# Performance work log

Hardware: AMD Instinct MI355X
Metric: run time of the kernel (lower is better)

The kernel has to match this reference:

```python
import jax, jax.numpy as jnp
import numpy as np

RANK_W, SP_W, ANS_W = 1.0, 1.0, 1.0


def _listmle(thres, scores, labels):
    # thres [B,1], scores [B,P], labels [B,P] with values in {-1,0,1}
    fs = jnp.concatenate([thres, scores], axis=1)                      # [B,K]
    fl = jnp.concatenate([jnp.full_like(thres, 0.5), labels], axis=1)  # [B,K]
    s = jnp.exp(fs) * (fl != -1.0).astype(fs.dtype)
    # rest[b,j] = sum_k s[b,k] * (fl[b,k] < fl[b,j])  (sorting in the original
    # is only used to enumerate; with the 0.5 break it reduces to masking
    # entries with label >= 0.5)
    less = (fl[:, None, :] < fl[:, :, None]).astype(fs.dtype)          # [B,j,k]
    rest = jnp.einsum('bjk,bk->bj', less, s)
    mask = fl >= 0.5
    den = jnp.where(mask, s + rest, 1.0)
    logp = jnp.where(mask, fs - jnp.log(den), 0.0)  # log(s_j/(s_j+rest)) with s_j=exp(fs_j)
    return -jnp.sum(logp)


def setup_inputs() -> dict:
    key = jax.random.key(0)
    B, S, H, NS, NP, A = 8, 4096, 1024, 64, 32, 8
    ks = jax.random.split(key, 12)
    sequence_output = jax.random.normal(ks[0], (B, S, H), jnp.float32)
    token_type_ids = jax.random.randint(ks[1], (B, S), 0, 2).astype(jnp.int32)
    # strictly increasing sentence boundaries; last 4 sentences padded with -1
    base = jnp.round(jnp.linspace(8, S - 8, NS + 1)).astype(jnp.int32)
    sent_starts = jnp.broadcast_to(base, (B, NS + 1)).copy()
    sent_starts = sent_starts.at[:, -4:].set(-1)
    para_starts = jnp.sort(jax.random.randint(ks[2], (B, NP), 0, S), axis=1).astype(jnp.int32)
    para_labels = jax.random.randint(ks[3], (B, NP), -1, 2).astype(jnp.float32)
    sp_sent_labels = jax.random.randint(ks[4], (B, NS), -1, 2).astype(jnp.float32)
    starts = jax.random.randint(ks[5], (B, A), -1, S).astype(jnp.int32)
    ends = jax.random.randint(ks[6], (B, A), -1, S).astype(jnp.int32)
    Wqa = jax.random.normal(ks[7], (H, 2), jnp.float32) * 0.02
    bqa = jnp.zeros((2,), jnp.float32)
    Wrank = jax.random.normal(ks[8], (H, 1), jnp.float32) * 0.02
    brank = jnp.zeros((1,), jnp.float32)
    Wsp = jax.random.normal(ks[9], (H, 1), jnp.float32) * 0.02
    bsp = jnp.zeros((1,), jnp.float32)
    return {"sequence_output": sequence_output, "token_type_ids": token_type_ids,
            "sent_starts": sent_starts, "para_starts": para_starts,
            "para_labels": para_labels, "sp_sent_labels": sp_sent_labels,
            "starts": starts, "ends": ends, "Wqa": Wqa, "bqa": bqa,
            "Wrank": Wrank, "brank": brank, "Wsp": Wsp, "bsp": bsp}


def reference(sequence_output, token_type_ids, sent_starts, para_starts,
              para_labels, sp_sent_labels, starts, ends,
              Wqa, bqa, Wrank, brank, Wsp, bsp):
    B, S, H = sequence_output.shape
    logits = sequence_output @ Wqa + bqa                               # [B,S,2]
    tt1 = token_type_ids == 1
    start_logits = jnp.where(tt1, logits[..., 0], -jnp.inf)
    end_logits = jnp.where(tt1, logits[..., 1], -jnp.inf)

    rank_thres = sequence_output[:, 0, :] @ Wrank + brank              # [B,1]
    sent_thres = sequence_output[:, 0, :] @ Wsp + bsp                  # [B,1]

    # ragged per-sentence mean pooling via prefix sums
    csum = jnp.concatenate([jnp.zeros((B, 1, H), sequence_output.dtype),
                            jnp.cumsum(sequence_output, axis=1)], axis=1)  # [B,S+1,H]
    st = sent_starts[:, :-1]
    en = sent_starts[:, 1:]
    valid = en != -1                                                   # [B,NS]
    st_c = jnp.clip(st, 0, S)
    en_c = jnp.maximum(jnp.clip(en, 0, S), st_c + 1)
    NS = st.shape[1]
    g_en = jnp.take_along_axis(csum, jnp.broadcast_to(en_c[:, :, None], (B, NS, H)), axis=1)
    g_st = jnp.take_along_axis(csum, jnp.broadcast_to(st_c[:, :, None], (B, NS, H)), axis=1)
    seg_mean = (g_en - g_st) / (en_c - st_c)[:, :, None].astype(sequence_output.dtype)
    sent_rep = jnp.where(valid[:, :, None], seg_mean, sequence_output[:, -1:, :])
    sp_score = (sent_rep @ Wsp + bsp)[..., 0]                          # [B,NS]

    NP = para_starts.shape[1]
    para_rep = jnp.take_along_axis(
        sequence_output, jnp.broadcast_to(para_starts[:, :, None].astype(jnp.int32), (B, NP, H)), axis=1)
    para_score = (para_rep @ Wrank + brank)[..., 0]                    # [B,NP]

    rank_loss = _listmle(rank_thres, para_score, para_labels)
    sp_loss = _listmle(sent_thres, sp_score, sp_sent_labels)

    ls_start = jax.nn.log_softmax(start_logits, axis=-1)
    ls_end = jax.nn.log_softmax(end_logits, axis=-1)

    def ce(ls, tgt):  # CrossEntropy with ignore_index=-1, reduction='none'
        safe = jnp.clip(tgt, 0, S - 1)
        nll = -jnp.take_along_axis(ls, safe, axis=1)
        return jnp.where(tgt == -1, 0.0, nll)

    loss_tensor = ce(ls_start, starts) + ce(ls_end, ends)              # [B,A]
    lp = -loss_tensor
    lp = jnp.where(lp == 0.0, -jnp.inf, lp)
    m = jnp.sum(jnp.exp(lp), axis=1)                                   # [B]
    pos = m > 0
    span_loss = -jnp.sum(jnp.where(pos, jnp.log(jnp.where(pos, m, 1.0)), 0.0))

    loss = rank_loss * RANK_W + span_loss * ANS_W + sp_loss * SP_W
    return (loss, rank_loss * RANK_W, sp_loss * SP_W)
```

## Files before the change

### kernel.cpp

```cpp
#include <hip/hip_runtime.h>
#include <math.h>

#define B 8
#define S 4096
#define H 1024
#define NSEG 64
#define NPARA 32
#define NA 8
#define BS (B * S)
#define ROWS_PER_BLK 16
#define BLKS_PER_B (S / ROWS_PER_BLK)
#define NBLK (B * BLKS_PER_B)

__device__ __forceinline__ float2 lse_merge(float2 A, float2 Bv)
{
    float m = fmaxf(A.x, Bv.x);
    float s = 0.f;
    if (A.y > 0.f)  s += A.y * expf(A.x - m);
    if (Bv.y > 0.f) s += Bv.y * expf(Bv.x - m);
    return make_float2(m, s);
}

__global__ __launch_bounds__(256) void dots_kernel(
    const float4* __restrict__ seq4,
    const float4* __restrict__ Wqa4,
    const float4* __restrict__ Wsp4,
    const float4* __restrict__ Wrank4,
    const int*    __restrict__ tt,
    const int*    __restrict__ sent_starts,
    float4* __restrict__ sc4,
    float4* __restrict__ lse_part,
    float4* __restrict__ segpart,
    float*  __restrict__ out)
{
    const int blk   = blockIdx.x;
    const int b     = blk >> 8;
    const int rbase = (blk & 255) * ROWS_PER_BLK;
    const int t     = threadIdx.x;
    const int w     = t >> 6, lane = t & 63;

    if (blk == 0 && t == 0) { out[0] = 0.f; out[1] = 0.f; out[2] = 0.f; }

    __shared__ int    ssh[NSEG + 1];
    __shared__ int    rowseg[ROWS_PER_BLK];
    __shared__ int    ttsh[ROWS_PER_BLK];
    __shared__ float4 lsep[4];
    __shared__ float2 wacc[4];
    __shared__ int    jlo_sh;

    float4 qA[4], qB[4], spv[4], rkv[4];
#pragma unroll
    for (int c = 0; c < 4; ++c) {
        const int ch = lane + 64 * c;
        qA[c]  = Wqa4[ch * 2];
        qB[c]  = Wqa4[ch * 2 + 1];
        spv[c] = Wsp4[ch];
        rkv[c] = Wrank4[ch];
    }

    if (t < NSEG + 1) ssh[t] = sent_starts[b * (NSEG + 1) + t];
    __syncthreads();
    if (t < ROWS_PER_BLK) {
        ttsh[t] = tt[b * S + rbase + t];
        const int r = rbase + t;
        int j = -1;
        for (int k = 0; k < NSEG; ++k) {
            int en = ssh[k + 1];
            if (en == -1) break;
            if (r >= ssh[k] && r < en) { j = k; break; }
        }
        rowseg[t] = j;
    }
    __syncthreads();
    if (t == 0) {
        int jl = -1;
        for (int i = 0; i < ROWS_PER_BLK; ++i)
            if (rowseg[i] >= 0) { jl = rowseg[i]; break; }
        jlo_sh = jl;
    }
    __syncthreads();
    const int jlo = jlo_sh;

    const float4* base = seq4 + (size_t)(b * S + rbase) * (H / 4);
    float mm = -INFINITY, ssum = 0.f;
    float segA = 0.f, segB = 0.f;

#pragma unroll
    for (int g = 0; g < 4; ++g) {
        const int lrow = g * 4 + w;
        const float4* rp = base + (size_t)lrow * (H / 4);
        float a0 = 0.f, a1 = 0.f, a2 = 0.f, a3 = 0.f;
#pragma unroll
        for (int c = 0; c < 4; ++c) {
            float4 v = rp[lane + 64 * c];
            a0 += v.x * qA[c].x + v.y * qA[c].z + v.z * qB[c].x + v.w * qB[c].z;
            a1 += v.x * qA[c].y + v.y * qA[c].w + v.z * qB[c].y + v.w * qB[c].w;
            a2 += v.x * spv[c].x + v.y * spv[c].y + v.z * spv[c].z + v.w * spv[c].w;
            a3 += v.x * rkv[c].x + v.y * rkv[c].y + v.z * rkv[c].z + v.w * rkv[c].w;
        }
        float u01 = (lane & 1) ? a0 : a1;
        float x01 = ((lane & 1) ? a1 : a0) + __shfl_xor(u01, 1);
        float u23 = (lane & 1) ? a2 : a3;
        float x23 = ((lane & 1) ? a3 : a2) + __shfl_xor(u23, 1);
        float uu  = (lane & 2) ? x01 : x23;
        float x   = ((lane & 2) ? x23 : x01) + __shfl_xor(uu, 2);
#pragma unroll
        for (int off = 4; off < 64; off <<= 1) x += __shfl_xor(x, off);
        if (ttsh[lrow] == 1) {
            float mn = fmaxf(mm, x);
            ssum = ssum * expf(mm - mn) + expf(x - mn);
            mm = mn;
        }
        const int j = rowseg[lrow];
        if (j >= 0) { if (j == jlo) segA += x; else segB += x; }
        if (lane < 4)
            ((float*)(sc4 + (size_t)b * S + rbase + lrow))[lane] = x;
    }

    {
        float mE = __shfl(mm, 1),   sE = __shfl(ssum, 1);
        float sa = __shfl(segA, 2), sb = __shfl(segB, 2);
        if (lane == 0) {
            lsep[w] = make_float4(mm, ssum, mE, sE);
            wacc[w] = make_float2(sa, sb);
        }
    }
    __syncthreads();
    if (t == 0) {
        float2 L0 = make_float2(lsep[0].x, lsep[0].y);
        float2 L1 = make_float2(lsep[0].z, lsep[0].w);
        float SA = wacc[0].x, SB = wacc[0].y;
#pragma unroll
        for (int i = 1; i < 4; ++i) {
            L0 = lse_merge(L0, make_float2(lsep[i].x, lsep[i].y));
            L1 = lse_merge(L1, make_float2(lsep[i].z, lsep[i].w));
            SA += wacc[i].x; SB += wacc[i].y;
        }
        lse_part[blk] = make_float4(L0.x, L0.y, L1.x, L1.y);
        segpart[blk]  = make_float4(__int_as_float(jlo), SA, SB, 0.f);
    }
}

__device__ __forceinline__ float blk_reduce1(float v, float* wred1, int t)
{
    const int lane = t & 63, w = t >> 6;
#pragma unroll
    for (int off = 32; off > 0; off >>= 1) v += __shfl_xor(v, off);
    if (lane == 0) wred1[w] = v;
    __syncthreads();
    float r = wred1[0] + wred1[1] + wred1[2] + wred1[3];
    __syncthreads();
    return r;
}

__device__ float listmle_block(const float* fs, const float* fl, float* se,
                               int n, float* wred1, int t)
{
    if (t < n) se[t] = (fl[t] != -1.0f) ? expf(fs[t]) : 0.0f;
    __syncthreads();
    float lp = 0.0f;
    if (t < n && fl[t] >= 0.5f) {
        float fj = fl[t];
        float rest = 0.0f;
        for (int k = 0; k < n; ++k)
            if (fl[k] < fj) rest += se[k];
        lp = fs[t] - logf(se[t] + rest);
    }
    float tot = blk_reduce1(lp, wred1, t);
    return -tot;
}

__global__ __launch_bounds__(256) void batch_kernel(
    const float4* __restrict__ sc4,
    const float4* __restrict__ lse_part,
    const float4* __restrict__ segpart,
    const int*    __restrict__ tt,
    const int*    __restrict__ sent_starts,
    const int*    __restrict__ para_starts,
    const float*  __restrict__ para_labels,
    const float*  __restrict__ sp_labels,
    const int*    __restrict__ starts,
    const int*    __restrict__ ends,
    float* __restrict__ out)
{
    const int b = blockIdx.x;
    const int t = threadIdx.x;
    const int lane = t & 63, w = t >> 6;

    __shared__ float4 lsew[4];
    __shared__ float  segsum[NSEG + 2];
    __shared__ int    ssh[NSEG + 1];
    __shared__ float  wred1[4];
    __shared__ float  fsb[1 + NSEG], flb[1 + NSEG], seb[1 + NSEG];
    __shared__ float  lse_sh[2];

    const float4* sb  = sc4 + (size_t)b * S;
    const int*    ttb = tt + b * S;

    if (t < NSEG + 2) segsum[t] = 0.f;
    if (t < NSEG + 1) ssh[t] = sent_starts[b * (NSEG + 1) + t];
    __syncthreads();

    {
        float4 P = lse_part[(size_t)b * BLKS_PER_B + t];
        float2 L0 = make_float2(P.x, P.y);
        float2 L1 = make_float2(P.z, P.w);
#pragma unroll
        for (int off = 32; off > 0; off >>= 1) {
            float2 O0 = make_float2(__shfl_xor(L0.x, off), __shfl_xor(L0.y, off));
            float2 O1 = make_float2(__shfl_xor(L1.x, off), __shfl_xor(L1.y, off));
            L0 = lse_merge(L0, O0);
            L1 = lse_merge(L1, O1);
        }
        if (lane == 0) lsew[w] = make_float4(L0.x, L0.y, L1.x, L1.y);

        float4 SP = segpart[(size_t)b * BLKS_PER_B + t];
        int jl = __float_as_int(SP.x);
        if (jl >= 0) {
            atomicAdd(&segsum[jl], SP.y);
            atomicAdd(&segsum[jl + 1], SP.z);
        }
    }
    __syncthreads();
    if (t == 0) {
        float2 M0 = make_float2(lsew[0].x, lsew[0].y);
        float2 M1 = make_float2(lsew[0].z, lsew[0].w);
#pragma unroll
        for (int i = 1; i < 4; ++i) {
            M0 = lse_merge(M0, make_float2(lsew[i].x, lsew[i].y));
            M1 = lse_merge(M1, make_float2(lsew[i].z, lsew[i].w));
        }
        lse_sh[0] = M0.x + logf(M0.y);
        lse_sh[1] = M1.x + logf(M1.y);
    }

    if (t == 0) { fsb[0] = sb[0].z; flb[0] = 0.5f; }
    if (t < NSEG) {
        int st = ssh[t];
        int en = ssh[t + 1];
        float score;
        if (en != -1) {
            int stc = min(max(st, 0), S);
            int enc = max(min(max(en, 0), S), stc + 1);
            score = segsum[t] / (float)(enc - stc);
        } else {
            score = sb[S - 1].z;
        }
        fsb[1 + t] = score;
        flb[1 + t] = sp_labels[b * NSEG + t];
    }
    __syncthreads();
    float sp_loss_b = listmle_block(fsb, flb, seb, 1 + NSEG, wred1, t);

    if (t == 0) { fsb[0] = sb[0].w; flb[0] = 0.5f; }
    if (t < NPARA) {
        int ps = para_starts[b * NPARA + t];
        fsb[1 + t] = sb[ps].w;
        flb[1 + t] = para_labels[b * NPARA + t];
    }
    __syncthreads();
    float rank_loss_b = listmle_block(fsb, flb, seb, 1 + NPARA, wred1, t);

    float e_a = 0.f;
    if (t < NA) {
        const float lse0 = lse_sh[0], lse1 = lse_sh[1];
        int tsv = starts[b * NA + t];
        int tev = ends[b * NA + t];
        float lt = 0.f;
        if (tsv != -1) {
            int sf = min(max(tsv, 0), S - 1);
            float sl = (ttb[sf] == 1) ? sb[sf].x : -INFINITY;
            lt += -(sl - lse0);
        }
        if (tev != -1) {
            int sf = min(max(tev, 0), S - 1);
            float el = (ttb[sf] == 1) ? sb[sf].y : -INFINITY;
            lt += -(el - lse1);
        }
        float lp = -lt;
        e_a = (lp == 0.0f) ? 0.f : expf(lp);
    }
#pragma unroll
    for (int off = 4; off > 0; off >>= 1) e_a += __shfl_xor(e_a, off, 8);
    if (t == 0) {
        float logm = (e_a > 0.f) ? logf(e_a) : 0.f;
        atomicAdd(out + 0, rank_loss_b + sp_loss_b - logm);
        atomicAdd(out + 1, rank_loss_b);
        atomicAdd(out + 2, sp_loss_b);
    }
}

extern "C" void kernel_launch(void* const* d_in, const int* in_sizes, int n_in,
                              void* d_out, int out_size, void* d_ws, size_t ws_size,
                              hipStream_t stream)
{
    const float* seq         = (const float*)d_in[0];
    const int*   tt          = (const int*)  d_in[1];
    const int*   sent_starts = (const int*)  d_in[2];
    const int*   para_starts = (const int*)  d_in[3];
    const float* para_labels = (const float*)d_in[4];
    const float* sp_labels   = (const float*)d_in[5];
    const int*   starts      = (const int*)  d_in[6];
    const int*   ends        = (const int*)  d_in[7];
    const float* Wqa         = (const float*)d_in[8];
    const float* Wrank       = (const float*)d_in[10];
    const float* Wsp         = (const float*)d_in[12];

    float*  out      = (float*)d_out;
    float4* sc4      = (float4*)d_ws;
    float4* lse_part = sc4 + (size_t)BS;
    float4* segpart  = lse_part + NBLK;

    dots_kernel<<<NBLK, 256, 0, stream>>>((const float4*)seq,
                                          (const float4*)Wqa,
                                          (const float4*)Wsp,
                                          (const float4*)Wrank,
                                          tt, sent_starts,
                                          sc4, lse_part, segpart, out);
    batch_kernel<<<B, 256, 0, stream>>>(sc4, lse_part, segpart, tt, sent_starts,
                                        para_starts, para_labels, sp_labels,
                                        starts, ends, out);
}
```

Baseline: 42.07 us.

## Stage rows through LDS with async global_load_lds triple-buffered pipeline

Doubles rows per block to 32 and has each wavefront stream its 8 rows into a per-wave 3-slot LDS ring using direct global-to-LDS loads, overlapping loads of upcoming rows with the dot-product compute on the current row via explicit vmcnt waits. Score stores are batched at the end, and the batch kernel is adjusted to the halved number of partial blocks. This targets memory latency in the bandwidth-bound reduction over the 128 MB input. It costs 48 KB of LDS per block, which limits occupancy, and relies on hand-counted vmcnt values being correct.

```diff
diff --git a/kernel.cpp b/kernel.cpp
--- a/kernel.cpp
+++ b/kernel.cpp
@@ -8,9 +8,16 @@
 #define NPARA 32
 #define NA 8
 #define BS (B * S)
-#define ROWS_PER_BLK 16
+#define ROWS_PER_BLK 32
 #define BLKS_PER_B (S / ROWS_PER_BLK)
 #define NBLK (B * BLKS_PER_B)
+
+__device__ __forceinline__ void gload_lds16(const float4* g, float4* l)
+{
+    __builtin_amdgcn_global_load_lds(
+        (const __attribute__((address_space(1))) void*)g,
+        (__attribute__((address_space(3))) void*)l, 16, 0, 0);
+}
 
 __device__ __forceinline__ float2 lse_merge(float2 A, float2 Bv)
 {
@@ -21,7 +28,7 @@
     return make_float2(m, s);
 }
 
-__global__ __launch_bounds__(256) void dots_kernel(
+__global__ __launch_bounds__(256, 3) void dots_kernel(
     const float4* __restrict__ seq4,
     const float4* __restrict__ Wqa4,
     const float4* __restrict__ Wsp4,
@@ -34,13 +41,14 @@
     float*  __restrict__ out)
 {
     const int blk   = blockIdx.x;
-    const int b     = blk >> 8;
-    const int rbase = (blk & 255) * ROWS_PER_BLK;
+    const int b     = blk >> 7;
+    const int rbase = (blk & 127) * ROWS_PER_BLK;
     const int t     = threadIdx.x;
     const int w     = t >> 6, lane = t & 63;
 
     if (blk == 0 && t == 0) { out[0] = 0.f; out[1] = 0.f; out[2] = 0.f; }
 
+    __shared__ float4 ring[4][3][256];
     __shared__ int    ssh[NSEG + 1];
     __shared__ int    rowseg[ROWS_PER_BLK];
     __shared__ int    ttsh[ROWS_PER_BLK];
@@ -84,37 +92,78 @@
     const float4* base = seq4 + (size_t)(b * S + rbase) * (H / 4);
     float mm = -INFINITY, ssum = 0.f;
     float segA = 0.f, segB = 0.f;
-
-#pragma unroll
-    for (int g = 0; g < 4; ++g) {
-        const int lrow = g * 4 + w;
-        const float4* rp = base + (size_t)lrow * (H / 4);
-        float a0 = 0.f, a1 = 0.f, a2 = 0.f, a3 = 0.f;
-#pragma unroll
-        for (int c = 0; c < 4; ++c) {
-            float4 v = rp[lane + 64 * c];
-            a0 += v.x * qA[c].x + v.y * qA[c].z + v.z * qB[c].x + v.w * qB[c].z;
-            a1 += v.x * qA[c].y + v.y * qA[c].w + v.z * qB[c].y + v.w * qB[c].w;
-            a2 += v.x * spv[c].x + v.y * spv[c].y + v.z * spv[c].z + v.w * spv[c].w;
-            a3 += v.x * rkv[c].x + v.y * rkv[c].y + v.z * rkv[c].z + v.w * rkv[c].w;
-        }
-        float u01 = (lane & 1) ? a0 : a1;
-        float x01 = ((lane & 1) ? a1 : a0) + __shfl_xor(u01, 1);
-        float u23 = (lane & 1) ? a2 : a3;
-        float x23 = ((lane & 1) ? a3 : a2) + __shfl_xor(u23, 1);
-        float uu  = (lane & 2) ? x01 : x23;
-        float x   = ((lane & 2) ? x23 : x01) + __shfl_xor(uu, 2);
-#pragma unroll
-        for (int off = 4; off < 64; off <<= 1) x += __shfl_xor(x, off);
-        if (ttsh[lrow] == 1) {
-            float mn = fmaxf(mm, x);
-            ssum = ssum * expf(mm - mn) + expf(x - mn);
-            mm = mn;
-        }
-        const int j = rowseg[lrow];
-        if (j >= 0) { if (j == jlo) segA += x; else segB += x; }
-        if (lane < 4)
-            ((float*)(sc4 + (size_t)b * S + rbase + lrow))[lane] = x;
+    float res[8];
+
+#define STAGE(r, buf)                                                         \
+    {                                                                         \
+        asm volatile("" ::: "memory");                                        \
+        const float4* gs = base + (size_t)(w * 8 + (r)) * 256;                \
+        float4* ld = &ring[w][buf][0];                                        \
+        gload_lds16(gs +   0 + lane, ld +   0);                               \
+        gload_lds16(gs +  64 + lane, ld +  64);                               \
+        gload_lds16(gs + 128 + lane, ld + 128);                               \
+        gload_lds16(gs + 192 + lane, ld + 192);                               \
+    }
+
+#define WAITVM(n) asm volatile("s_waitcnt vmcnt(" #n ")" ::: "memory")
+
+#define FMA_C(c)                                                              \
+    {   float4 v = rp[lane + 64 * (c)];                                       \
+        a0 += v.x*qA[c].x  + v.y*qA[c].z  + v.z*qB[c].x  + v.w*qB[c].z;       \
+        a1 += v.x*qA[c].y  + v.y*qA[c].w  + v.z*qB[c].y  + v.w*qB[c].w;       \
+        a2 += v.x*spv[c].x + v.y*spv[c].y + v.z*spv[c].z + v.w*spv[c].w;      \
+        a3 += v.x*rkv[c].x + v.y*rkv[c].y + v.z*rkv[c].z + v.w*rkv[c].w; }
+
+#define COMPUTE(r, buf)                                                       \
+    {                                                                         \
+        const int lrow = w * 8 + (r);                                         \
+        const float4* rp = &ring[w][buf][0];                                  \
+        float a0 = 0.f, a1 = 0.f, a2 = 0.f, a3 = 0.f;                         \
+        FMA_C(0) FMA_C(1) FMA_C(2) FMA_C(3)                                   \
+        float u01 = (lane & 1) ? a0 : a1;                                     \
+        float x01 = ((lane & 1) ? a1 : a0) + __shfl_xor(u01, 1);              \
+        float u23 = (lane & 1) ? a2 : a3;                                     \
+        float x23 = ((lane & 1) ? a3 : a2) + __shfl_xor(u23, 1);              \
+        float uu  = (lane & 2) ? x01 : x23;                                   \
+        float x   = ((lane & 2) ? x23 : x01) + __shfl_xor(uu, 2);             \
+        x += __shfl_xor(x, 4); x += __shfl_xor(x, 8);                         \
+        x += __shfl_xor(x, 16); x += __shfl_xor(x, 32);                       \
+        if (ttsh[lrow] == 1) {                                                \
+            float mn = fmaxf(mm, x);                                          \
+            ssum = ssum * expf(mm - mn) + expf(x - mn);                       \
+            mm = mn;                                                          \
+        }                                                                     \
+        const int j = rowseg[lrow];                                           \
+        if (j >= 0) { if (j == jlo) segA += x; else segB += x; }              \
+        res[r] = x;                                                           \
+    }
+
+    STAGE(0, 0);
+    STAGE(1, 1);
+    STAGE(2, 2);
+    WAITVM(8);  COMPUTE(0, 0);
+    STAGE(3, 0);
+    WAITVM(8);  COMPUTE(1, 1);
+    STAGE(4, 1);
+    WAITVM(8);  COMPUTE(2, 2);
+    STAGE(5, 2);
+    WAITVM(8);  COMPUTE(3, 0);
+    STAGE(6, 0);
+    WAITVM(8);  COMPUTE(4, 1);
+    STAGE(7, 1);
+    WAITVM(8);  COMPUTE(5, 2);
+    WAITVM(4);  COMPUTE(6, 0);
+    WAITVM(0);  COMPUTE(7, 1);
+
+#undef STAGE
+#undef WAITVM
+#undef FMA_C
+#undef COMPUTE
+
+    if (lane < 4) {
+#pragma unroll
+        for (int r = 0; r < 8; ++r)
+            ((float*)(sc4 + (size_t)b * S + rbase + w * 8 + r))[lane] = res[r];
     }
 
     {
@@ -187,7 +236,7 @@
     const int t = threadIdx.x;
     const int lane = t & 63, w = t >> 6;
 
-    __shared__ float4 lsew[4];
+    __shared__ float4 lsew[2];
     __shared__ float  segsum[NSEG + 2];
     __shared__ int    ssh[NSEG + 1];
     __shared__ float  wred1[4];
@@ -201,7 +250,7 @@
     if (t < NSEG + 1) ssh[t] = sent_starts[b * (NSEG + 1) + t];
     __syncthreads();
 
-    {
+    if (t < BLKS_PER_B) {
         float4 P = lse_part[(size_t)b * BLKS_PER_B + t];
         float2 L0 = make_float2(P.x, P.y);
         float2 L1 = make_float2(P.z, P.w);
@@ -223,13 +272,10 @@
     }
     __syncthreads();
     if (t == 0) {
-        float2 M0 = make_float2(lsew[0].x, lsew[0].y);
-        float2 M1 = make_float2(lsew[0].z, lsew[0].w);
-#pragma unroll
-        for (int i = 1; i < 4; ++i) {
-            M0 = lse_merge(M0, make_float2(lsew[i].x, lsew[i].y));
-            M1 = lse_merge(M1, make_float2(lsew[i].z, lsew[i].w));
-        }
+        float2 M0 = lse_merge(make_float2(lsew[0].x, lsew[0].y),
+                              make_float2(lsew[1].x, lsew[1].y));
+        float2 M1 = lse_merge(make_float2(lsew[0].z, lsew[0].w),
+                              make_float2(lsew[1].z, lsew[1].w));
         lse_sh[0] = M0.x + logf(M0.y);
         lse_sh[1] = M1.x + logf(M1.y);
     }
```

Result: slower. 46.29 us (+10.0%).

## Split each row across the whole block and batch row loads before reducing

Applied to the files above, without the earlier changes.

The dot kernel now has each of the 256 threads own one float4 column chunk for all 16 rows, rather than one wave per row with four chunks per lane. All 16 row loads are issued in two batches of 8 to raise memory-level parallelism. Partial sums are combined through shared memory, and a single wave then computes the per-block log-sum-exp and segment sums with shuffles. Weight registers shrink, and launch bounds ask for 3 blocks per SM, but holding 16 float4 accumulators raises register pressure.

```diff
diff --git a/kernel.cpp b/kernel.cpp
--- a/kernel.cpp
+++ b/kernel.cpp
@@ -21,7 +21,7 @@
     return make_float2(m, s);
 }
 
-__global__ __launch_bounds__(256) void dots_kernel(
+__global__ __launch_bounds__(256, 3) void dots_kernel(
     const float4* __restrict__ seq4,
     const float4* __restrict__ Wqa4,
     const float4* __restrict__ Wsp4,
@@ -41,22 +41,16 @@
 
     if (blk == 0 && t == 0) { out[0] = 0.f; out[1] = 0.f; out[2] = 0.f; }
 
-    __shared__ int    ssh[NSEG + 1];
-    __shared__ int    rowseg[ROWS_PER_BLK];
-    __shared__ int    ttsh[ROWS_PER_BLK];
-    __shared__ float4 lsep[4];
-    __shared__ float2 wacc[4];
-    __shared__ int    jlo_sh;
-
-    float4 qA[4], qB[4], spv[4], rkv[4];
-#pragma unroll
-    for (int c = 0; c < 4; ++c) {
-        const int ch = lane + 64 * c;
-        qA[c]  = Wqa4[ch * 2];
-        qB[c]  = Wqa4[ch * 2 + 1];
-        spv[c] = Wsp4[ch];
-        rkv[c] = Wrank4[ch];
-    }
+    __shared__ float part[ROWS_PER_BLK][16];
+    __shared__ int   ssh[NSEG + 1];
+    __shared__ int   rowseg[ROWS_PER_BLK];
+    __shared__ int   ttsh[ROWS_PER_BLK];
+    __shared__ int   jlo_sh;
+
+    const float4 qA = Wqa4[2 * t];
+    const float4 qB = Wqa4[2 * t + 1];
+    const float4 sp = Wsp4[t];
+    const float4 rk = Wrank4[t];
 
     if (t < NSEG + 1) ssh[t] = sent_starts[b * (NSEG + 1) + t];
     __syncthreads();
@@ -81,63 +75,73 @@
     __syncthreads();
     const int jlo = jlo_sh;
 
-    const float4* base = seq4 + (size_t)(b * S + rbase) * (H / 4);
-    float mm = -INFINITY, ssum = 0.f;
-    float segA = 0.f, segB = 0.f;
-
-#pragma unroll
-    for (int g = 0; g < 4; ++g) {
-        const int lrow = g * 4 + w;
-        const float4* rp = base + (size_t)lrow * (H / 4);
-        float a0 = 0.f, a1 = 0.f, a2 = 0.f, a3 = 0.f;
-#pragma unroll
-        for (int c = 0; c < 4; ++c) {
-            float4 v = rp[lane + 64 * c];
-            a0 += v.x * qA[c].x + v.y * qA[c].z + v.z * qB[c].x + v.w * qB[c].z;
-            a1 += v.x * qA[c].y + v.y * qA[c].w + v.z * qB[c].y + v.w * qB[c].w;
-            a2 += v.x * spv[c].x + v.y * spv[c].y + v.z * spv[c].z + v.w * spv[c].w;
-            a3 += v.x * rkv[c].x + v.y * rkv[c].y + v.z * rkv[c].z + v.w * rkv[c].w;
-        }
-        float u01 = (lane & 1) ? a0 : a1;
-        float x01 = ((lane & 1) ? a1 : a0) + __shfl_xor(u01, 1);
-        float u23 = (lane & 1) ? a2 : a3;
-        float x23 = ((lane & 1) ? a3 : a2) + __shfl_xor(u23, 1);
+    const float4* base = seq4 + (size_t)(b * S + rbase) * (H / 4) + t;
+
+    float4 acc[ROWS_PER_BLK];
+    float4 v[8];
+#pragma unroll
+    for (int r = 0; r < 8; ++r) v[r] = base[(size_t)r * (H / 4)];
+#pragma unroll
+    for (int r = 0; r < 8; ++r) {
+        float4 x = v[r], a;
+        a.x = x.x * qA.x + x.y * qA.z + x.z * qB.x + x.w * qB.z;
+        a.y = x.x * qA.y + x.y * qA.w + x.z * qB.y + x.w * qB.w;
+        a.z = x.x * sp.x + x.y * sp.y + x.z * sp.z + x.w * sp.w;
+        a.w = x.x * rk.x + x.y * rk.y + x.z * rk.z + x.w * rk.w;
+        acc[r] = a;
+    }
+#pragma unroll
+    for (int r = 0; r < 8; ++r) v[r] = base[(size_t)(r + 8) * (H / 4)];
+#pragma unroll
+    for (int r = 0; r < 8; ++r) {
+        float4 x = v[r], a;
+        a.x = x.x * qA.x + x.y * qA.z + x.z * qB.x + x.w * qB.z;
+        a.y = x.x * qA.y + x.y * qA.w + x.z * qB.y + x.w * qB.w;
+        a.z = x.x * sp.x + x.y * sp.y + x.z * sp.z + x.w * sp.w;
+        a.w = x.x * rk.x + x.y * rk.y + x.z * rk.z + x.w * rk.w;
+        acc[r + 8] = a;
+    }
+
+#pragma unroll
+    for (int r = 0; r < ROWS_PER_BLK; ++r) {
+        float4 a = acc[r];
+        float u01 = (lane & 1) ? a.x : a.y;
+        float x01 = ((lane & 1) ? a.y : a.x) + __shfl_xor(u01, 1);
+        float u23 = (lane & 1) ? a.z : a.w;
+        float x23 = ((lane & 1) ? a.w : a.z) + __shfl_xor(u23, 1);
         float uu  = (lane & 2) ? x01 : x23;
         float x   = ((lane & 2) ? x23 : x01) + __shfl_xor(uu, 2);
-#pragma unroll
-        for (int off = 4; off < 64; off <<= 1) x += __shfl_xor(x, off);
-        if (ttsh[lrow] == 1) {
-            float mn = fmaxf(mm, x);
-            ssum = ssum * expf(mm - mn) + expf(x - mn);
-            mm = mn;
-        }
-        const int j = rowseg[lrow];
-        if (j >= 0) { if (j == jlo) segA += x; else segB += x; }
-        if (lane < 4)
-            ((float*)(sc4 + (size_t)b * S + rbase + lrow))[lane] = x;
-    }
-
-    {
-        float mE = __shfl(mm, 1),   sE = __shfl(ssum, 1);
-        float sa = __shfl(segA, 2), sb = __shfl(segB, 2);
+        x += __shfl_xor(x, 4);  x += __shfl_xor(x, 8);
+        x += __shfl_xor(x, 16); x += __shfl_xor(x, 32);
+        if (lane < 4) part[r][w * 4 + lane] = x;
+    }
+    __syncthreads();
+
+    if (w == 0) {
+        const int r = lane >> 2, k = lane & 3;
+        float x = part[r][k] + part[r][4 + k] + part[r][8 + k] + part[r][12 + k];
+        ((float*)(sc4 + (size_t)b * S + rbase))[lane] = x;
+
+        const bool inc = (ttsh[r] == 1);
+        float mx = inc ? x : -INFINITY;
+#pragma unroll
+        for (int off = 4; off < 64; off <<= 1) mx = fmaxf(mx, __shfl_xor(mx, off));
+        float ex = inc ? expf(x - mx) : 0.f;
+        const int j = rowseg[r];
+        float sA = (j >= 0 && j == jlo) ? x : 0.f;
+        float sB = (j >= 0 && j != jlo) ? x : 0.f;
+#pragma unroll
+        for (int off = 4; off < 64; off <<= 1) {
+            ex += __shfl_xor(ex, off);
+            sA += __shfl_xor(sA, off);
+            sB += __shfl_xor(sB, off);
+        }
+        float m1  = __shfl(mx, 1), s1 = __shfl(ex, 1);
+        float sa2 = __shfl(sA, 2), sb2 = __shfl(sB, 2);
         if (lane == 0) {
-            lsep[w] = make_float4(mm, ssum, mE, sE);
-            wacc[w] = make_float2(sa, sb);
-        }
-    }
-    __syncthreads();
-    if (t == 0) {
-        float2 L0 = make_float2(lsep[0].x, lsep[0].y);
-        float2 L1 = make_float2(lsep[0].z, lsep[0].w);
-        float SA = wacc[0].x, SB = wacc[0].y;
-#pragma unroll
-        for (int i = 1; i < 4; ++i) {
-            L0 = lse_merge(L0, make_float2(lsep[i].x, lsep[i].y));
-            L1 = lse_merge(L1, make_float2(lsep[i].z, lsep[i].w));
-            SA += wacc[i].x; SB += wacc[i].y;
-        }
-        lse_part[blk] = make_float4(L0.x, L0.y, L1.x, L1.y);
-        segpart[blk]  = make_float4(__int_as_float(jlo), SA, SB, 0.f);
+            lse_part[blk] = make_float4(mx, ex, m1, s1);
+            segpart[blk]  = make_float4(__int_as_float(jlo), sa2, sb2, 0.f);
+        }
     }
 }
 
```

Measured after the change: 43.62 us. 3.7% more time.
